# Optimization experiments

Measured on AMD Instinct MI355X. Metric: run time of the kernel, lower is better.

## Reference

```python
import jax, jax.numpy as jnp
import numpy as np

N = 40000; E = 400000; F = 16; H = 8; C = 64; R1 = 40; R2 = 40; MAXR = 60
NEG_SLOPE = 0.2


def setup_inputs() -> dict:
    key = jax.random.key(0)
    ks = jax.random.split(key, 16)
    inp = {}
    inp['x1'] = jax.random.normal(ks[0], (N, F), dtype=jnp.float32)
    inp['edge_index1'] = jax.random.randint(ks[1], (2, E), 0, N)
    inp['edge_attr1'] = jax.random.normal(ks[2], (E, 4), dtype=jnp.float32)
    inp['route_vec1'] = jax.random.randint(ks[3], (N,), 0, R1)
    inp['n_routes1'] = R1
    inp['x2'] = jax.random.normal(ks[4], (N, F), dtype=jnp.float32)
    inp['edge_index2'] = jax.random.randint(ks[5], (2, E), 0, N)
    inp['edge_attr2'] = jax.random.normal(ks[6], (E, 4), dtype=jnp.float32)
    inp['route_vec2'] = jax.random.randint(ks[7], (N,), 0, R2)
    inp['n_routes2'] = R2
    # GATConv params (glorot-ish scaling)
    inp['W_gat'] = jax.random.normal(ks[8], (F, H * C), dtype=jnp.float32) / np.sqrt(F)
    inp['att_src'] = jax.random.normal(ks[9], (H, C), dtype=jnp.float32) / np.sqrt(C)
    inp['att_dst'] = jax.random.normal(ks[10], (H, C), dtype=jnp.float32) / np.sqrt(C)
    inp['bias_gat'] = jnp.zeros((H * C,), dtype=jnp.float32)
    # route combination head: Linear(2*H*C -> MAXR+1)
    D = 2 * H * C
    inp['W_head'] = jax.random.normal(ks[11], (D, MAXR + 1), dtype=jnp.float32) / np.sqrt(D)
    inp['b_head'] = jnp.zeros((MAXR + 1,), dtype=jnp.float32)
    return inp


def _gat_conv(x, edge_index, W, att_src, att_dst, bias):
    """PyG GATConv (concat=True, add_self_loops=True, eval-mode dropout, edge_attr ignored)."""
    n = x.shape[0]
    loops = jnp.arange(n, dtype=edge_index.dtype)
    ei = jnp.concatenate([edge_index, jnp.stack([loops, loops])], axis=1)
    src, dst = ei[0], ei[1]
    h = (x @ W).reshape(n, H, C)                      # [N,H,C]
    a_s = jnp.sum(h * att_src, axis=-1)               # [N,H]
    a_d = jnp.sum(h * att_dst, axis=-1)               # [N,H]
    e = jax.nn.leaky_relu(a_s[src] + a_d[dst], NEG_SLOPE)   # [E',H]
    m = jax.ops.segment_max(e, dst, num_segments=n)   # stable softmax per dst node
    ex = jnp.exp(e - m[dst])
    denom = jax.ops.segment_sum(ex, dst, num_segments=n)
    alpha = ex / denom[dst]                           # [E',H]
    out = jax.ops.segment_sum(h[src] * alpha[:, :, None], dst, num_segments=n)  # [N,H,C]
    return out.reshape(n, H * C) + bias


def reference(x1, edge_index1, edge_attr1, route_vec1, n_routes1,
              x2, edge_index2, edge_attr2, route_vec2, n_routes2,
              W_gat, att_src, att_dst, bias_gat, W_head, b_head):
    # edge_attr is ignored: GATConv was built without edge_dim.
    emb1 = _gat_conv(x1, edge_index1, W_gat, att_src, att_dst, bias_gat)  # [N,H*C]
    emb2 = _gat_conv(x2, edge_index2, W_gat, att_src, att_dst, bias_gat)
    # one-hot(node->route).T @ emb  ==  segment_sum over routes
    agg1 = jax.ops.segment_sum(emb1, route_vec1, num_segments=n_routes1)  # [R1,H*C]
    agg2 = jax.ops.segment_sum(emb2, route_vec2, num_segments=n_routes2)  # [R2,H*C]
    a = jnp.broadcast_to(agg1[:, None, :], (n_routes1, n_routes2, H * C))
    b = jnp.broadcast_to(agg2[None, :, :], (n_routes1, n_routes2, H * C))
    pair = jnp.concatenate([a, b], axis=-1)                               # [R1,R2,2HC]
    full = pair @ W_head + b_head                                         # [R1,R2,MAXR+1]
    max_to_swap = min(n_routes1, n_routes2)
    logits = full[:n_routes1, :n_routes2, :max_to_swap - 1]
    probs = jax.nn.softmax(logits.reshape(-1), axis=-1).reshape(logits.shape)
    return probs
```

## Files before the change

kernel.cpp:

```cpp
#include <hip/hip_runtime.h>
#include <hip/hip_fp16.h>

#define NN 40000
#define NE 400000
#define NF 16
#define NH 8
#define NR 40
#define NK 39
#define NEG 0.2f
#define NBLK 157
#define NCH 16
#define NB 157
#define SLOT 3328
#define BPG 391
#define GAB 40

#define OFF_AS   0
#define OFF_AD   (OFF_AS + 2*NN*NH)
#define OFF_P    (OFF_AD + 2*NN*NH)
#define OFF_PART (OFF_P + 2*NR*NK)
#define OFF_S    (OFF_PART + 2*NR*NCH*128)
#define OFF_XH   (OFF_S + 2*NN*64)
#define OFF_INT  (OFF_XH + 2*NN*8)
#define IOFF_RHIST  0
#define IOFF_BCUR   (2*NR)
#define IOFF_RCUR   (2*NR + 2*NB)
#define IOFF_START  (IOFF_RCUR + 2*NR)
#define IOFF_DEG    (IOFF_START + 2*NN)
#define IOFF_NID    (IOFF_DEG + 2*NN)
#define IOFF_BINNED (IOFF_NID + 2*NN)
#define IOFF_SRC    (IOFF_BINNED + 2*NB*SLOT)

static __device__ __forceinline__ unsigned int f2bf(float v) {
    unsigned int x = __float_as_uint(v);
    return (x + 0x7FFFu + ((x >> 16) & 1u)) >> 16;
}
static __device__ __forceinline__ float bf2f(unsigned int u) {
    return __uint_as_float(u << 16);
}
static __device__ __forceinline__ unsigned int packh2(float a, float b) {
    __half2 hv = __floats2half2_rn(a, b);
    return *(unsigned int*)&hv;
}
static __device__ __forceinline__ float2 unpackh2(unsigned int u) {
    __half2 hv = *(__half2*)&u;
    return __half22float2(hv);
}

__global__ __launch_bounds__(512) void k_zero(int* __restrict__ p,
                                              int* __restrict__ srcs) {
    int i = threadIdx.x;
    if (i < 2 * NR + 2 * NB + 2 * NR) p[i] = 0;
    if (i == 0) srcs[2 * NB * SLOT] = 0;
}

__global__ __launch_bounds__(1024) void k_front(const float* __restrict__ x1,
                                                const float* __restrict__ x2,
                                                const int* __restrict__ rv1,
                                                const int* __restrict__ rv2,
                                                const int* __restrict__ ei1,
                                                const int* __restrict__ ei2,
                                                const float* __restrict__ W,
                                                const float* __restrict__ asrc,
                                                const float* __restrict__ adst,
                                                float* __restrict__ as_,
                                                float* __restrict__ ad_,
                                                unsigned int* __restrict__ xh,
                                                int* __restrict__ rhist,
                                                int* __restrict__ bcur,
                                                unsigned int* __restrict__ binned) {
    __shared__ float us[256];
    __shared__ int lh[NR];
    __shared__ int lhb[NB], lbb[NB];
    int tid = threadIdx.x;
    if (blockIdx.x < 2 * GAB) {
        if (tid < NR) lh[tid] = 0;
        if (tid < 256) {
            int tt = tid & 127;
            int f = tt >> 3, h = tt & 7;
            const float* av = (tid < 128 ? asrc : adst) + h * 64;
            const float* wrow = W + f * 512 + h * 64;
            float su = 0.f;
            for (int c = 0; c < 64; ++c) su += wrow[c] * av[c];
            us[tid] = su;
        }
        __syncthreads();
        int g = blockIdx.x / GAB;
        int n = (blockIdx.x - g * GAB) * 1024 + tid;
        if (n < NN) {
            const float* x = g ? x2 : x1;
            const int* rv = g ? rv2 : rv1;
            const float4* xp = (const float4*)(x + n * NF);
            float4 v0 = xp[0], v1 = xp[1], v2 = xp[2], v3 = xp[3];
            float xv[16] = {v0.x, v0.y, v0.z, v0.w, v1.x, v1.y, v1.z, v1.w,
                            v2.x, v2.y, v2.z, v2.w, v3.x, v3.y, v3.z, v3.w};
            int o = g * NN * NH + n * NH;
            for (int h = 0; h < NH; ++h) {
                float s1 = 0.f, s2 = 0.f;
                for (int f = 0; f < NF; ++f) {
                    s1 += xv[f] * us[f * 8 + h];
                    s2 += xv[f] * us[128 + f * 8 + h];
                }
                as_[o + h] = s1;
                ad_[o + h] = s2;
            }
            unsigned int* xo = xh + ((size_t)g * NN + n) * 8;
            #pragma unroll
            for (int p = 0; p < 8; ++p) xo[p] = packh2(xv[2 * p], xv[2 * p + 1]);
            atomicAdd(&lh[rv[n]], 1);
        }
        __syncthreads();
        if (tid < NR && lh[tid]) atomicAdd(&rhist[g * NR + tid], lh[tid]);
    } else {
        int bid = blockIdx.x - 2 * GAB;
        int g = bid >= BPG;
        int blk = bid - g * BPG;
        if (tid < NB) lhb[tid] = 0;
        __syncthreads();
        int e = blk * 1024 + tid;
        const int* ei = g ? ei2 : ei1;
        unsigned int v = 0;
        int bin = 0, lpos = 0;
        bool valid = (e < NE);
        if (valid) {
            unsigned int s = (unsigned int)ei[e];
            unsigned int dv = (unsigned int)ei[NE + e];
            v = (dv << 16) | s;
            bin = dv >> 8;
            lpos = atomicAdd(&lhb[bin], 1);
        }
        __syncthreads();
        if (tid < NB && lhb[tid]) lbb[tid] = atomicAdd(&bcur[g * NB + tid], lhb[tid]);
        __syncthreads();
        if (valid) {
            int p = lbb[bin] + lpos;
            if (p < SLOT) binned[(g * NB + bin) * SLOT + p] = v;
        }
    }
}

__global__ __launch_bounds__(256) void k_mid(const int* __restrict__ bcur,
                                             const unsigned int* __restrict__ binned,
                                             const int* __restrict__ rv1,
                                             const int* __restrict__ rv2,
                                             const int* __restrict__ rhist,
                                             int* __restrict__ rcur,
                                             int* __restrict__ start,
                                             int* __restrict__ deg,
                                             int* __restrict__ srcs,
                                             int* __restrict__ nid) {
    __shared__ unsigned int ed[SLOT];
    __shared__ int hist[256], scn[256];
    __shared__ int lh[NR], lbase[NR], rbase[NR];
    int tid = threadIdx.x;
    if (blockIdx.x < 2 * NB) {
        int gb = blockIdx.x;
        int g = gb >= NB;
        int b = gb - g * NB;
        int m = bcur[gb]; if (m > SLOT) m = SLOT;
        int base = gb * SLOT;
        for (int i = tid; i < m; i += 256) ed[i] = binned[base + i];
        hist[tid] = 0;
        __syncthreads();
        for (int i = tid; i < m; i += 256) atomicAdd(&hist[(ed[i] >> 16) & 255], 1);
        __syncthreads();
        int v = hist[tid];
        scn[tid] = v;
        __syncthreads();
        for (int off = 1; off < 256; off <<= 1) {
            int u = (tid >= off) ? scn[tid - off] : 0;
            __syncthreads();
            scn[tid] += u;
            __syncthreads();
        }
        int excl = scn[tid] - v;
        int d = b * 256 + tid;
        if (d < NN) { start[g * NN + d] = base + excl; deg[g * NN + d] = v; }
        hist[tid] = excl;
        __syncthreads();
        for (int i = tid; i < m; i += 256) {
            unsigned int e = ed[i];
            int ld = (e >> 16) & 255;
            int pos = atomicAdd(&hist[ld], 1);
            srcs[base + pos] = (int)(e & 0xffffu);
        }
    } else {
        int bid = blockIdx.x - 2 * NB;
        int g = bid / NBLK;
        int n = (bid - g * NBLK) * 256 + tid;
        const int* rv = g ? rv2 : rv1;
        if (tid < NR) lh[tid] = 0;
        __syncthreads();
        int r = 0, lpos = 0;
        bool valid = (n < NN);
        if (valid) { r = rv[n]; lpos = atomicAdd(&lh[r], 1); }
        if (tid == 0) {
            int run = 0;
            for (int rr = 0; rr < NR; ++rr) { rbase[rr] = run; run += rhist[g * NR + rr]; }
        }
        __syncthreads();
        if (tid < NR && lh[tid])
            lbase[tid] = rbase[tid] + atomicAdd(&rcur[g * NR + tid], lh[tid]);
        __syncthreads();
        if (valid) nid[g * NN + lbase[r] + lpos] = n;
    }
}

__global__ __launch_bounds__(256) void k_gather(const int* __restrict__ start,
                                                const int* __restrict__ deg,
                                                const int* __restrict__ srcs,
                                                const float* __restrict__ as_,
                                                const float* __restrict__ ad_,
                                                const unsigned int* __restrict__ xh,
                                                unsigned int* __restrict__ sb) {
    int bid = blockIdx.x;
    int xcd = bid & 7;
    int g = xcd >> 2;
    int lblk = (xcd & 3) * 2500 + (bid >> 3);
    int d = lblk * 4 + (threadIdx.x >> 6);
    int idx = g * NN + d;
    const float* asg = as_ + (size_t)g * NN * NH;
    const unsigned int* xg = xh + (size_t)g * NN * 8;
    int lane = threadIdx.x & 63;
    int h = lane >> 3, q = lane & 7;
    float adv = ad_[(size_t)g * NN * NH + d * NH + h];
    float e0 = asg[d * NH + h] + adv;
    e0 = (e0 > 0.f) ? e0 : NEG * e0;
    float w0 = __expf(e0);
    float2 xv = unpackh2(xg[d * 8 + q]);
    float wsum = w0;
    float ax = w0 * xv.x, ay = w0 * xv.y;
    int base = __builtin_amdgcn_readfirstlane(start[idx]);
    int dg   = __builtin_amdgcn_readfirstlane(deg[idx]);
    int nb = (dg + 7) >> 3;
    for (int b = 0; b < nb; ++b) {
        int off = base + b * 8;
        int lim = dg - b * 8;
        int aq = (q < lim) ? off + q : base;
        int sq = srcs[aq];
        float ev = asg[sq * NH + h] + adv;
        ev = (ev > 0.f) ? ev : NEG * ev;
        float wq = (q < lim) ? __expf(ev) : 0.f;
        int sB = __shfl(sq, lane >> 3);
        unsigned int xu = xg[sB * 8 + q];
        #pragma unroll
        for (int j = 0; j < 8; ++j) {
            float wj = __shfl(wq, (lane & 56) | j);
            unsigned int xj = (unsigned int)__shfl((int)xu, (j << 3) | q);
            float2 xf = unpackh2(xj);
            wsum += wj;
            ax += wj * xf.x;
            ay += wj * xf.y;
        }
    }
    float inv = 1.0f / wsum;
    unsigned int pk = (f2bf(ay * inv) << 16) | f2bf(ax * inv);
    sb[(size_t)idx * 64 + lane] = pk;
}

__global__ __launch_bounds__(256) void k_rnode(const int* __restrict__ rhist,
                                               const int* __restrict__ nid,
                                               const unsigned int* __restrict__ sb,
                                               float* __restrict__ part) {
    __shared__ float red[4][128];
    __shared__ int sseg[2];
    int bid = blockIdx.x;
    int xcd = bid & 7;
    int g = xcd >> 2;
    int rch = (xcd & 3) * (NR * NCH / 4) + (bid >> 3);
    int r = rch / NCH, ch = rch - r * NCH;
    if (threadIdx.x == 0) {
        int acc = 0;
        for (int rr = 0; rr < r; ++rr) acc += rhist[g * NR + rr];
        sseg[0] = acc;
        sseg[1] = rhist[g * NR + r];
    }
    __syncthreads();
    int seg0 = sseg[0], dgr = sseg[1];
    int csz = (dgr + NCH - 1) / NCH;
    int a = seg0 + ch * csz;
    int b = seg0 + dgr; { int bb = a + csz; if (bb < b) b = bb; }
    int ln = threadIdx.x >> 6, c = threadIdx.x & 63;
    const int* np = nid + g * NN;
    const unsigned int* sg = sb + (size_t)g * NN * 64;
    float sx = 0.f, sy = 0.f;
    for (int i = a + ln; i < b; i += 4) {
        int n = np[i];
        unsigned int pk = sg[(size_t)n * 64 + c];
        sx += bf2f(pk & 0xffffu);
        sy += bf2f(pk >> 16);
    }
    red[ln][c * 2] = sx;
    red[ln][c * 2 + 1] = sy;
    __syncthreads();
    int tid = threadIdx.x;
    if (tid < 128) {
        float s = red[0][tid] + red[1][tid] + red[2][tid] + red[3][tid];
        part[((g * NR + r) * NCH + ch) * 128 + tid] = s;
    }
}

__global__ __launch_bounds__(256) void k_head(const float* __restrict__ part,
                                              const int* __restrict__ rhist,
                                              const float* __restrict__ W,
                                              const float* __restrict__ bias,
                                              const float* __restrict__ Wh,
                                              float* __restrict__ P) {
    __shared__ float trow[128];
    __shared__ float aggL[512];
    __shared__ float scnt;
    int g = blockIdx.x / NR, i = blockIdx.x - g * NR;
    int tid = threadIdx.x;
    if (tid < 128) {
        const float* pp = part + ((g * NR + i) * NCH) * 128 + tid;
        float s = 0.f;
        for (int ch = 0; ch < NCH; ++ch) s += pp[ch * 128];
        trow[tid] = s;
    }
    if (tid == 0) scnt = (float)rhist[g * NR + i];
    __syncthreads();
    for (int hc = tid; hc < 512; hc += 256) {
        int h = hc >> 6;
        float acc = scnt * bias[hc];
        const float* tp = trow + h * 16;
        for (int f = 0; f < 16; ++f) acc += tp[f] * W[f * 512 + hc];
        aggL[hc] = acc;
    }
    __syncthreads();
    if (tid < 4 * NK) {
        int k = tid >> 2, qq = tid & 3;
        const float* wp = Wh + (size_t)(g * 512 + qq * 128) * 61 + k;
        const float* ap = aggL + qq * 128;
        float acc = 0.f;
        for (int d = 0; d < 128; ++d) acc += ap[d] * wp[d * 61];
        acc += __shfl_down(acc, 1);
        acc += __shfl_down(acc, 2);
        if (qq == 0) P[(g * NR + i) * NK + k] = acc;
    }
}

__global__ __launch_bounds__(1024) void k_final(const float* __restrict__ P,
                                                const float* __restrict__ bh,
                                                float* __restrict__ out) {
    __shared__ float p1[NR * NK], p2[NR * NK];
    __shared__ float ak[NK], ck[NK], s1k[NK], s2k[NK];
    __shared__ float fk[NK];
    int tid = threadIdx.x;
    for (int i = tid; i < NR * NK; i += 1024) { p1[i] = P[i]; p2[i] = P[NR * NK + i]; }
    __syncthreads();
    if (tid < 2 * NK) {
        int k = (tid < NK) ? tid : tid - NK;
        float* pp = (tid < NK) ? p1 : p2;
        float a = -3.0e38f;
        for (int i = 0; i < NR; ++i) a = fmaxf(a, pp[i * NK + k]);
        float s = 0.f;
        for (int i = 0; i < NR; ++i) {
            float e = __expf(pp[i * NK + k] - a);
            pp[i * NK + k] = e;
            s += e;
        }
        if (tid < NK) { ak[k] = a; s1k[k] = s; }
        else          { ck[k] = a; s2k[k] = s; }
    }
    __syncthreads();
    if (tid == 0) {
        float M = -3.0e38f;
        float mk[NK];
        for (int k = 0; k < NK; ++k) {
            mk[k] = ak[k] + ck[k] + bh[k];
            M = fmaxf(M, mk[k]);
        }
        float den = 0.f;
        for (int k = 0; k < NK; ++k) den += s1k[k] * s2k[k] * __expf(mk[k] - M);
        float invden = 1.0f / den;
        for (int k = 0; k < NK; ++k) fk[k] = __expf(mk[k] - M) * invden;
    }
    __syncthreads();
    const int TOT = NR * NR * NK;
    for (int idx = tid; idx < TOT; idx += 1024) {
        int i = idx / (NR * NK);
        int r = idx - i * (NR * NK);
        int j = r / NK;
        int k = r - j * NK;
        out[idx] = p1[i * NK + k] * p2[j * NK + k] * fk[k];
    }
}

extern "C" void kernel_launch(void* const* d_in, const int* in_sizes, int n_in,
                              void* d_out, int out_size, void* d_ws, size_t ws_size,
                              hipStream_t stream) {
    const float* x1   = (const float*)d_in[0];
    const int*   ei1  = (const int*)d_in[1];
    const int*   rv1  = (const int*)d_in[3];
    const float* x2   = (const float*)d_in[5];
    const int*   ei2  = (const int*)d_in[6];
    const int*   rv2  = (const int*)d_in[8];
    const float* Wg   = (const float*)d_in[10];
    const float* asrc = (const float*)d_in[11];
    const float* adst = (const float*)d_in[12];
    const float* bias = (const float*)d_in[13];
    const float* Wh   = (const float*)d_in[14];
    const float* bh   = (const float*)d_in[15];
    float* out = (float*)d_out;
    float* ws  = (float*)d_ws;

    float* as_  = ws + OFF_AS;
    float* ad_  = ws + OFF_AD;
    float* P    = ws + OFF_P;
    float* part = ws + OFF_PART;
    unsigned int* sb = (unsigned int*)(ws + OFF_S);
    unsigned int* xh = (unsigned int*)(ws + OFF_XH);
    int* ibase  = (int*)(ws + OFF_INT);
    int* rhist  = ibase + IOFF_RHIST;
    int* bcur   = ibase + IOFF_BCUR;
    int* rcur   = ibase + IOFF_RCUR;
    int* start  = ibase + IOFF_START;
    int* deg    = ibase + IOFF_DEG;
    int* nid    = ibase + IOFF_NID;
    unsigned int* binned = (unsigned int*)(ibase + IOFF_BINNED);
    int* srcs   = ibase + IOFF_SRC;

    k_zero<<<1, 512, 0, stream>>>(rhist, srcs);
    k_front<<<2 * GAB + 2 * BPG, 1024, 0, stream>>>(x1, x2, rv1, rv2, ei1, ei2,
                                                    Wg, asrc, adst, as_, ad_, xh,
                                                    rhist, bcur, binned);
    k_mid<<<2 * NB + 2 * NBLK, 256, 0, stream>>>(bcur, binned, rv1, rv2, rhist,
                                                 rcur, start, deg, srcs, nid);
    k_gather<<<2 * NN / 4, 256, 0, stream>>>(start, deg, srcs, as_, ad_, xh, sb);
    k_rnode<<<2 * NR * NCH, 256, 0, stream>>>(rhist, nid, sb, part);
    k_head<<<2 * NR, 256, 0, stream>>>(part, rhist, Wg, bias, Wh, P);
    k_final<<<1, 1024, 0, stream>>>(P, bh, out);
}
```

Measured before the change: 107.5 us.

## Vectorize edge binning, pack gather weights in half2, widen route-node loads

Edge binning now has each thread process two edges through int2 loads, which halves the front-stage block count. The gather loop packs pairs of attention weights into half2, pre-scaled by 1/16 to avoid fp16 overflow, and loads each source index directly rather than shuffling it. This reduces shuffles per neighbour but lowers weight precision. The route-node reduction reads uint2 per lane, splits each wave into two halves over nodes, and combines the halves with a xor-shuffle.

```diff
diff --git a/kernel.cpp b/kernel.cpp
--- a/kernel.cpp
+++ b/kernel.cpp
@@ -12,8 +12,9 @@
 #define NCH 16
 #define NB 157
 #define SLOT 3328
-#define BPG 391
+#define BPG2 196
 #define GAB 40
+#define WS 0.0625f
 
 #define OFF_AS   0
 #define OFF_AD   (OFF_AS + 2*NN*NH)
@@ -113,28 +114,33 @@
         if (tid < NR && lh[tid]) atomicAdd(&rhist[g * NR + tid], lh[tid]);
     } else {
         int bid = blockIdx.x - 2 * GAB;
-        int g = bid >= BPG;
-        int blk = bid - g * BPG;
+        int g = bid >= BPG2;
+        int blk = bid - g * BPG2;
         if (tid < NB) lhb[tid] = 0;
         __syncthreads();
-        int e = blk * 1024 + tid;
+        int e2 = blk * 1024 + tid;
         const int* ei = g ? ei2 : ei1;
-        unsigned int v = 0;
-        int bin = 0, lpos = 0;
-        bool valid = (e < NE);
+        unsigned int v0 = 0, v1 = 0;
+        int bin0 = 0, bin1 = 0, lp0 = 0, lp1 = 0;
+        bool valid = (e2 < NE / 2);
         if (valid) {
-            unsigned int s = (unsigned int)ei[e];
-            unsigned int dv = (unsigned int)ei[NE + e];
-            v = (dv << 16) | s;
-            bin = dv >> 8;
-            lpos = atomicAdd(&lhb[bin], 1);
+            int2 sv = *(const int2*)&ei[2 * e2];
+            int2 dv = *(const int2*)&ei[NE + 2 * e2];
+            v0 = ((unsigned int)dv.x << 16) | (unsigned int)sv.x;
+            v1 = ((unsigned int)dv.y << 16) | (unsigned int)sv.y;
+            bin0 = (unsigned int)dv.x >> 8;
+            bin1 = (unsigned int)dv.y >> 8;
+            lp0 = atomicAdd(&lhb[bin0], 1);
+            lp1 = atomicAdd(&lhb[bin1], 1);
         }
         __syncthreads();
         if (tid < NB && lhb[tid]) lbb[tid] = atomicAdd(&bcur[g * NB + tid], lhb[tid]);
         __syncthreads();
         if (valid) {
-            int p = lbb[bin] + lpos;
-            if (p < SLOT) binned[(g * NB + bin) * SLOT + p] = v;
+            int p0 = lbb[bin0] + lp0;
+            int p1 = lbb[bin1] + lp1;
+            if (p0 < SLOT) binned[(g * NB + bin0) * SLOT + p0] = v0;
+            if (p1 < SLOT) binned[(g * NB + bin1) * SLOT + p1] = v1;
         }
     }
 }
@@ -223,10 +229,11 @@
     const unsigned int* xg = xh + (size_t)g * NN * 8;
     int lane = threadIdx.x & 63;
     int h = lane >> 3, q = lane & 7;
+    int a8 = lane >> 3;
     float adv = ad_[(size_t)g * NN * NH + d * NH + h];
     float e0 = asg[d * NH + h] + adv;
     e0 = (e0 > 0.f) ? e0 : NEG * e0;
-    float w0 = __expf(e0);
+    float w0 = __expf(e0) * WS;
     float2 xv = unpackh2(xg[d * 8 + q]);
     float wsum = w0;
     float ax = w0 * xv.x, ay = w0 * xv.y;
@@ -237,20 +244,26 @@
         int off = base + b * 8;
         int lim = dg - b * 8;
         int aq = (q < lim) ? off + q : base;
+        int aA = (a8 < lim) ? off + a8 : base;
         int sq = srcs[aq];
+        int sA = srcs[aA];
         float ev = asg[sq * NH + h] + adv;
         ev = (ev > 0.f) ? ev : NEG * ev;
-        float wq = (q < lim) ? __expf(ev) : 0.f;
-        int sB = __shfl(sq, lane >> 3);
-        unsigned int xu = xg[sB * 8 + q];
+        float wq = (q < lim) ? __expf(ev) * WS : 0.f;
+        float wpart = __shfl_xor(wq, 1);
+        unsigned int wpair = (q & 1) ? packh2(wpart, wq) : packh2(wq, wpart);
+        unsigned int xu = xg[sA * 8 + q];
         #pragma unroll
-        for (int j = 0; j < 8; ++j) {
-            float wj = __shfl(wq, (lane & 56) | j);
-            unsigned int xj = (unsigned int)__shfl((int)xu, (j << 3) | q);
-            float2 xf = unpackh2(xj);
-            wsum += wj;
-            ax += wj * xf.x;
-            ay += wj * xf.y;
+        for (int p = 0; p < 4; ++p) {
+            unsigned int wp = (unsigned int)__shfl((int)wpair, (lane & 56) | (p << 1));
+            float2 wf = unpackh2(wp);
+            unsigned int xj0 = (unsigned int)__shfl((int)xu, ((p << 1) << 3) | q);
+            unsigned int xj1 = (unsigned int)__shfl((int)xu, (((p << 1) | 1) << 3) | q);
+            float2 x0 = unpackh2(xj0);
+            float2 x1 = unpackh2(xj1);
+            wsum += wf.x + wf.y;
+            ax += wf.x * x0.x + wf.y * x1.x;
+            ay += wf.x * x0.y + wf.y * x1.y;
         }
     }
     float inv = 1.0f / wsum;
@@ -280,18 +293,29 @@
     int csz = (dgr + NCH - 1) / NCH;
     int a = seg0 + ch * csz;
     int b = seg0 + dgr; { int bb = a + csz; if (bb < b) b = bb; }
-    int ln = threadIdx.x >> 6, c = threadIdx.x & 63;
+    int ln = threadIdx.x >> 6;
+    int lane = threadIdx.x & 63;
+    int par = lane >> 5;
+    int p = lane & 31;
     const int* np = nid + g * NN;
     const unsigned int* sg = sb + (size_t)g * NN * 64;
-    float sx = 0.f, sy = 0.f;
-    for (int i = a + ln; i < b; i += 4) {
+    float sx0 = 0.f, sy0 = 0.f, sx1 = 0.f, sy1 = 0.f;
+    for (int i = a + ln * 2 + par; i < b; i += 8) {
         int n = np[i];
-        unsigned int pk = sg[(size_t)n * 64 + c];
-        sx += bf2f(pk & 0xffffu);
-        sy += bf2f(pk >> 16);
-    }
-    red[ln][c * 2] = sx;
-    red[ln][c * 2 + 1] = sy;
+        uint2 pk = *(const uint2*)&sg[(size_t)n * 64 + p * 2];
+        sx0 += bf2f(pk.x & 0xffffu); sy0 += bf2f(pk.x >> 16);
+        sx1 += bf2f(pk.y & 0xffffu); sy1 += bf2f(pk.y >> 16);
+    }
+    sx0 += __shfl_xor(sx0, 32);
+    sy0 += __shfl_xor(sy0, 32);
+    sx1 += __shfl_xor(sx1, 32);
+    sy1 += __shfl_xor(sy1, 32);
+    if (par == 0) {
+        red[ln][p * 4 + 0] = sx0;
+        red[ln][p * 4 + 1] = sy0;
+        red[ln][p * 4 + 2] = sx1;
+        red[ln][p * 4 + 3] = sy1;
+    }
     __syncthreads();
     int tid = threadIdx.x;
     if (tid < 128) {
@@ -421,9 +445,9 @@
     int* srcs   = ibase + IOFF_SRC;
 
     k_zero<<<1, 512, 0, stream>>>(rhist, srcs);
-    k_front<<<2 * GAB + 2 * BPG, 1024, 0, stream>>>(x1, x2, rv1, rv2, ei1, ei2,
-                                                    Wg, asrc, adst, as_, ad_, xh,
-                                                    rhist, bcur, binned);
+    k_front<<<2 * GAB + 2 * BPG2, 1024, 0, stream>>>(x1, x2, rv1, rv2, ei1, ei2,
+                                                     Wg, asrc, adst, as_, ad_, xh,
+                                                     rhist, bcur, binned);
     k_mid<<<2 * NB + 2 * NBLK, 256, 0, stream>>>(bcur, binned, rv1, rv2, rhist,
                                                  rcur, start, deg, srcs, nid);
     k_gather<<<2 * NN / 4, 256, 0, stream>>>(start, deg, srcs, as_, ad_, xh, sb);
```

Result: faster. 97.83 us, median of 2 (-9.0%).
